# Kernel optimization log

Measured on AMD Instinct MI355X. Metric: run time of the kernel, lower is better.

The kernel has to match this reference:

```python
import jax, jax.numpy as jnp
import numpy as np

C, D, N = 1000, 512, 200_000  # classes, feature dim, total ragged samples
LAM = 1.0  # self.lam

def setup_inputs() -> dict:
    key = jax.random.key(0)
    k1, k2, k3, k4, k5 = jax.random.split(key, 5)
    w_preds = jax.random.normal(k1, (C, D), jnp.float32)
    w_stars = jax.random.normal(k2, (C, D), jnp.float32)
    feats = jax.random.normal(k3, (N, D), jnp.float32)        # flattened ragged x
    ys = jnp.sign(jax.random.normal(k4, (N,), jnp.float32))   # +/-1 labels y[idx]
    seg_ids = jax.random.randint(k5, (N,), 0, C)              # which class each sample belongs to
    return {"w_preds": w_preds, "w_stars": w_stars, "feats": feats, "ys": ys, "seg_ids": seg_ids}

def reference(w_preds, w_stars, feats, ys, seg_ids):
    # MSE with reduction='sum'
    reg_loss = jnp.sum((w_preds - w_stars) ** 2)
    # perf_loss = sum_n (1 - y_n * <w_preds[class(n)], x_n>)
    dots = jnp.einsum('nd,nd->n', feats, w_preds[seg_ids])
    perf_loss = jnp.sum(1.0 - ys * dots)
    return reg_loss + LAM * perf_loss
```

## Files before the change

kernel.cpp:

```cpp
#include <hip/hip_runtime.h>


#define BLOCK 256
#define GRID  2048
#define CHUNK 25

typedef float vf4 __attribute__((ext_vector_type(4)));

__global__ void init_out(float* out, float n_const) {
    out[0] = n_const;
}

__device__ __forceinline__ float dot8(vf4 a0, vf4 a1, vf4 u0, vf4 u1) {
    return a0.x * u0.x + a0.y * u0.y + a0.z * u0.z + a0.w * u0.w
         + a1.x * u1.x + a1.y * u1.y + a1.z * u1.z + a1.w * u1.w;
}

__global__ __launch_bounds__(BLOCK) void mrn_loss_kernel(
    const float* __restrict__ wp,
    const float* __restrict__ wst,
    const float* __restrict__ feats,
    const float* __restrict__ ys,
    const int*   __restrict__ seg,
    float* __restrict__ out,
    int N)
{
    const int tid      = blockIdx.x * BLOCK + threadIdx.x;
    const int nthreads = gridDim.x * BLOCK;

    float acc_a = 0.0f;
    float acc_b = 0.0f;

    {
        const int REG4 = (1000 * 512) / 4;
        const vf4* wp4 = (const vf4*)wp;
        const vf4* ws4 = (const vf4*)wst;
        for (int i = tid; i < REG4; i += nthreads) {
            vf4 a = wp4[i];
            vf4 b = ws4[i];
            vf4 d = a - b;
            acc_a += d.x * d.x + d.y * d.y + d.z * d.z + d.w * d.w;
        }
    }

    {
        const int lane = threadIdx.x & 63;
        const int wave = __builtin_amdgcn_readfirstlane(tid >> 6);
        const int base = wave * CHUNK;

        if (base < N) {
            const int cnt = min(CHUNK, N - base);

            int   myseg = 0;
            float myy   = 0.0f;
            if (lane < cnt) {
                myseg = seg[base + lane];
                myy   = ys[base + lane];
            }

            const vf4* f4 = (const vf4*)feats + (size_t)base * 128;

            if (cnt == CHUNK) {
                #pragma unroll 5
                for (int j = 0; j < CHUNK; ++j) {
                    const int   c = __builtin_amdgcn_readlane(myseg, j);
                    const float y = __int_as_float(
                        __builtin_amdgcn_readlane(__float_as_int(myy), j));

                    const vf4* fr = f4 + (size_t)j * 128;
                    const vf4* wr = (const vf4*)(wp + (size_t)c * 512);

                    vf4 a0 = __builtin_nontemporal_load(fr + lane);
                    vf4 a1 = __builtin_nontemporal_load(fr + lane + 64);
                    vf4 u0 = wr[lane];
                    vf4 u1 = wr[lane + 64];

                    const float d = dot8(a0, a1, u0, u1);
                    if (j & 1) acc_b -= y * d;
                    else       acc_a -= y * d;
                }
            } else {
                for (int j = 0; j < cnt; ++j) {
                    const int   c = __shfl(myseg, j, 64);
                    const float y = __shfl(myy,   j, 64);
                    const vf4* fr = f4 + (size_t)j * 128;
                    const vf4* wr = (const vf4*)(wp + (size_t)c * 512);
                    vf4 a0 = __builtin_nontemporal_load(fr + lane);
                    vf4 a1 = __builtin_nontemporal_load(fr + lane + 64);
                    vf4 u0 = wr[lane];
                    vf4 u1 = wr[lane + 64];
                    acc_a -= y * dot8(a0, a1, u0, u1);
                }
            }
        }
    }

    float acc = acc_a + acc_b;
    for (int off = 32; off > 0; off >>= 1)
        acc += __shfl_down(acc, off, 64);

    __shared__ float sacc[BLOCK / 64];
    const int lane = threadIdx.x & 63;
    const int wid  = threadIdx.x >> 6;
    if (lane == 0) sacc[wid] = acc;
    __syncthreads();

    if (threadIdx.x == 0) {
        float b = sacc[0] + sacc[1] + sacc[2] + sacc[3];
        atomicAdd(out, b);
    }
}

extern "C" void kernel_launch(void* const* d_in, const int* in_sizes, int n_in,
                              void* d_out, int out_size, void* d_ws, size_t ws_size,
                              hipStream_t stream) {
    const float* wp    = (const float*)d_in[0];
    const float* wst   = (const float*)d_in[1];
    const float* feats = (const float*)d_in[2];
    const float* ys    = (const float*)d_in[3];
    const int*   seg   = (const int*)d_in[4];
    float* out = (float*)d_out;

    const int N = in_sizes[3];

    init_out<<<1, 1, 0, stream>>>(out, (float)N);
    mrn_loss_kernel<<<GRID, BLOCK, 0, stream>>>(wp, wst, feats, ys, seg, out, N);
}
```

Before: 81.95 us.

## Halve grid, add grid-stride chunk loop, replace atomics with two-pass reduction

The grid shrinks from 2048 to 1024 blocks, the per-wave chunk grows to 49 samples, and a grid-stride loop covers the remaining rows so each wave handles more samples. Per-block partial sums are written to workspace and reduced by a small second kernel instead of atomicAdd, which also gives a deterministic sum. The tail loop uses readlane instead of shfl. The costs are an extra kernel launch and fewer waves in flight to hide memory latency.

```diff
diff --git a/kernel.cpp b/kernel.cpp
--- a/kernel.cpp
+++ b/kernel.cpp
@@ -2,13 +2,23 @@
 
 
 #define BLOCK 256
-#define GRID  2048
-#define CHUNK 25
+#define GRID  1024
+#define CHUNK 49
+#define NWAVES (GRID * (BLOCK / 64))
 
 typedef float vf4 __attribute__((ext_vector_type(4)));
 
-__global__ void init_out(float* out, float n_const) {
-    out[0] = n_const;
+__global__ void init_out(float* out, float n_const) { out[0] = n_const; }
+
+__global__ void final_reduce(const float* __restrict__ part, float* __restrict__ out,
+                             float n_const) {
+    float a = 0.0f;
+    for (int i = threadIdx.x; i < GRID; i += 256) a += part[i];
+    for (int off = 32; off > 0; off >>= 1) a += __shfl_down(a, off, 64);
+    __shared__ float s[4];
+    if ((threadIdx.x & 63) == 0) s[threadIdx.x >> 6] = a;
+    __syncthreads();
+    if (threadIdx.x == 0) out[0] = n_const + s[0] + s[1] + s[2] + s[3];
 }
 
 __device__ __forceinline__ float dot8(vf4 a0, vf4 a1, vf4 u0, vf4 u1) {
@@ -16,17 +26,18 @@
          + a1.x * u1.x + a1.y * u1.y + a1.z * u1.z + a1.w * u1.w;
 }
 
-__global__ __launch_bounds__(BLOCK) void mrn_loss_kernel(
+__global__ __launch_bounds__(BLOCK, 4) void mrn_loss_kernel(
     const float* __restrict__ wp,
     const float* __restrict__ wst,
     const float* __restrict__ feats,
     const float* __restrict__ ys,
     const int*   __restrict__ seg,
+    float* __restrict__ blockout,
     float* __restrict__ out,
     int N)
 {
     const int tid      = blockIdx.x * BLOCK + threadIdx.x;
-    const int nthreads = gridDim.x * BLOCK;
+    const int nthreads = GRID * BLOCK;
 
     float acc_a = 0.0f;
     float acc_b = 0.0f;
@@ -46,9 +57,8 @@
     {
         const int lane = threadIdx.x & 63;
         const int wave = __builtin_amdgcn_readfirstlane(tid >> 6);
-        const int base = wave * CHUNK;
 
-        if (base < N) {
+        for (int base = wave * CHUNK; base < N; base += NWAVES * CHUNK) {
             const int cnt = min(CHUNK, N - base);
 
             int   myseg = 0;
@@ -61,7 +71,7 @@
             const vf4* f4 = (const vf4*)feats + (size_t)base * 128;
 
             if (cnt == CHUNK) {
-                #pragma unroll 5
+                #pragma unroll 3
                 for (int j = 0; j < CHUNK; ++j) {
                     const int   c = __builtin_amdgcn_readlane(myseg, j);
                     const float y = __int_as_float(
@@ -81,8 +91,9 @@
                 }
             } else {
                 for (int j = 0; j < cnt; ++j) {
-                    const int   c = __shfl(myseg, j, 64);
-                    const float y = __shfl(myy,   j, 64);
+                    const int   c = __builtin_amdgcn_readlane(myseg, j);
+                    const float y = __int_as_float(
+                        __builtin_amdgcn_readlane(__float_as_int(myy), j));
                     const vf4* fr = f4 + (size_t)j * 128;
                     const vf4* wr = (const vf4*)(wp + (size_t)c * 512);
                     vf4 a0 = __builtin_nontemporal_load(fr + lane);
@@ -107,7 +118,8 @@
 
     if (threadIdx.x == 0) {
         float b = sacc[0] + sacc[1] + sacc[2] + sacc[3];
-        atomicAdd(out, b);
+        if (blockout) blockout[blockIdx.x] = b;
+        else          atomicAdd(out, b);
     }
 }
 
@@ -123,6 +135,14 @@
 
     const int N = in_sizes[3];
 
-    init_out<<<1, 1, 0, stream>>>(out, (float)N);
-    mrn_loss_kernel<<<GRID, BLOCK, 0, stream>>>(wp, wst, feats, ys, seg, out, N);
+    if (ws_size >= GRID * sizeof(float)) {
+        float* part = (float*)d_ws;
+        mrn_loss_kernel<<<GRID, BLOCK, 0, stream>>>(wp, wst, feats, ys, seg,
+                                                    part, nullptr, N);
+        final_reduce<<<1, 256, 0, stream>>>(part, out, (float)N);
+    } else {
+        init_out<<<1, 1, 0, stream>>>(out, (float)N);
+        mrn_loss_kernel<<<GRID, BLOCK, 0, stream>>>(wp, wst, feats, ys, seg,
+                                                    nullptr, out, N);
+    }
 }
```

New measurement: 78.74 us, median of 2. -3.9%, faster.
